# Kernel tuning notes

Hardware: AMD Instinct MI355X
Metric: run time of the kernel (lower is better)

The kernel has to match this reference:

```python
import jax, jax.numpy as jnp
import numpy as np

D_OUT, D_IN, R, N_TOK = 4096, 4096, 16, 8192

def setup_inputs() -> dict:
    key = jax.random.key(0)
    k1, k2, k3, k4 = jax.random.split(key, 4)
    x = jax.random.normal(k1, (N_TOK, D_IN), dtype=jnp.float32)
    W = jax.random.normal(k2, (D_OUT, D_IN), dtype=jnp.float32) * (1.0 / np.sqrt(D_IN))
    bias = jax.random.normal(k3, (D_OUT,), dtype=jnp.float32) * 0.02
    lora_B = jnp.zeros((D_OUT, R), dtype=jnp.float32)  # torch init: zeros
    lora_A = jax.random.normal(k4, (R, D_IN), dtype=jnp.float32) / R  # torch init: randn / r
    lora_scale = jnp.float32(1.0)
    return {"x": x, "W": W, "bias": bias, "lora_B": lora_B, "lora_A": lora_A, "lora_scale": lora_scale}

def reference(x, W, bias, lora_B, lora_A, lora_scale):
    # Faithful to torch: weight = W + scale * B @ A; out = x @ weight.T + bias
    weight = W + lora_scale * (lora_B @ lora_A)  # [d_out, d_in]
    return jnp.einsum('ni,oi->no', x, weight) + bias
```

## Files before the change

kernel.cpp:

```cpp
#include <hip/hip_runtime.h>
#include <stdint.h>
#include <stddef.h>

#define M_TOK 8192
#define N_OUT 4096
#define K_IN  4096
#define R_LORA 16
#define BM 128
#define BN 256
#define BK 32

#define WEFF_BLOCKS ((K_IN / 1024) * (N_OUT / 32))
#define CAST_BLOCKS ((M_TOK * K_IN) / (8 * 256))

typedef __bf16 bf16_t;
typedef __bf16 bf16x4 __attribute__((ext_vector_type(4)));
typedef __bf16 bf16x8 __attribute__((ext_vector_type(8)));
typedef float floatx4 __attribute__((ext_vector_type(4)));

__device__ inline void async_copy16(const bf16_t* g, bf16_t* l) {
  __builtin_amdgcn_global_load_lds(
      (__attribute__((address_space(1))) void*)(uintptr_t)(const void*)g,
      (__attribute__((address_space(3))) void*)l,
      16, 0, 0);
}

__global__ __launch_bounds__(256) void prep_fused(
    const float* __restrict__ x, bf16_t* __restrict__ xb,
    const float* __restrict__ W, const float* __restrict__ lB,
    const float* __restrict__ lA, const float* __restrict__ scale_p,
    bf16_t* __restrict__ wb) {
  const int b = blockIdx.x;
  if (b < WEFF_BLOCKS) {
    const int kbase = (b & 3) * 1024 + threadIdx.x * 4;
    const int o0    = (b >> 2) * 32;
    const float scale = *scale_p;

    float4 areg[R_LORA];
#pragma unroll
    for (int r = 0; r < R_LORA; ++r)
      areg[r] = *(const float4*)(lA + (size_t)r * K_IN + kbase);

    for (int oo = 0; oo < 32; ++oo) {
      const int o = o0 + oo;
      float4 w = *(const float4*)(W + (size_t)o * K_IN + kbase);
      float a0 = w.x, a1 = w.y, a2 = w.z, a3 = w.w;
#pragma unroll
      for (int r = 0; r < R_LORA; ++r) {
        float bb = lB[(size_t)o * R_LORA + r] * scale;
        a0 += bb * areg[r].x; a1 += bb * areg[r].y;
        a2 += bb * areg[r].z; a3 += bb * areg[r].w;
      }
      bf16x4 v;
      v[0] = (bf16_t)a0; v[1] = (bf16_t)a1; v[2] = (bf16_t)a2; v[3] = (bf16_t)a3;
      *(bf16x4*)(wb + (size_t)o * K_IN + kbase) = v;
    }
  } else {
    const size_t t = (size_t)(b - WEFF_BLOCKS) * 256 + threadIdx.x;
    const float4* xp = (const float4*)x + t * 2;
    float4 a0 = xp[0];
    float4 a1 = xp[1];
    bf16x8 v;
    v[0] = (bf16_t)a0.x; v[1] = (bf16_t)a0.y; v[2] = (bf16_t)a0.z; v[3] = (bf16_t)a0.w;
    v[4] = (bf16_t)a1.x; v[5] = (bf16_t)a1.y; v[6] = (bf16_t)a1.z; v[7] = (bf16_t)a1.w;
    *(bf16x8*)(xb + t * 8) = v;
  }
}

__global__ __launch_bounds__(256, 2) void gemm_bt(const bf16_t* __restrict__ A,
                                                  const bf16_t* __restrict__ Bw,
                                                  const float* __restrict__ bias,
                                                  float* __restrict__ C) {
  __shared__ bf16_t sA[2 * BM * BK];
  __shared__ bf16_t sB[2 * BN * BK];

  const int tid  = threadIdx.x;
  const int wave = tid >> 6;
  const int lane = tid & 63;
  const int lr   = lane & 15;
  const int quad = lane >> 4;
  const int bm = blockIdx.y * BM;
  const int bn = blockIdx.x * BN;
  const int wm = (wave >> 1) * 64;
  const int wn = (wave & 1) * 128;

  const bf16_t* gA[2];
  const bf16_t* gB[4];
  bf16_t* lA0[2];
  bf16_t* lB0[4];
#pragma unroll
  for (int i = 0; i < 2; ++i) {
    int s = i * 256 + wave * 64 + lane;
    int row = s >> 2;
    int q = ((s & 3) - (s >> 3)) & 3;
    gA[i] = A + (size_t)(bm + row) * K_IN + q * 8;
    lA0[i] = sA + (size_t)(i * 256 + wave * 64) * 8;
  }
#pragma unroll
  for (int i = 0; i < 4; ++i) {
    int s = i * 256 + wave * 64 + lane;
    int row = s >> 2;
    int q = ((s & 3) - (s >> 3)) & 3;
    gB[i] = Bw + (size_t)(bn + row) * K_IN + q * 8;
    lB0[i] = sB + (size_t)(i * 256 + wave * 64) * 8;
  }

  const int cofs = ((quad + (lr >> 1)) & 3) * 8;
  const bf16_t* fA[4];
  const bf16_t* fB[8];
#pragma unroll
  for (int i = 0; i < 4; ++i) fA[i] = sA + (wm + i * 16 + lr) * 32 + cofs;
#pragma unroll
  for (int j = 0; j < 8; ++j) fB[j] = sB + (wn + j * 16 + lr) * 32 + cofs;

  floatx4 acc[4][8];
#pragma unroll
  for (int i = 0; i < 4; ++i)
#pragma unroll
    for (int j = 0; j < 8; ++j) acc[i][j] = {0.f, 0.f, 0.f, 0.f};

#define STAGE(buf_ofsA, buf_ofsB)                                   \
  do {                                                              \
    async_copy16(gA[0], lA0[0] + (buf_ofsA));                       \
    async_copy16(gA[1], lA0[1] + (buf_ofsA));                       \
    async_copy16(gB[0], lB0[0] + (buf_ofsB));                       \
    async_copy16(gB[1], lB0[1] + (buf_ofsB));                       \
    async_copy16(gB[2], lB0[2] + (buf_ofsB));                       \
    async_copy16(gB[3], lB0[3] + (buf_ofsB));                       \
    gA[0] += BK; gA[1] += BK;                                       \
    gB[0] += BK; gB[1] += BK; gB[2] += BK; gB[3] += BK;             \
  } while (0)

#define COMPUTE(buf_ofsA, buf_ofsB)                                                   \
  do {                                                                                \
    bf16x8 a[4], b[8];                                                                \
    _Pragma("unroll") for (int i = 0; i < 4; ++i)                                     \
        a[i] = *(const bf16x8*)(fA[i] + (buf_ofsA));                                  \
    _Pragma("unroll") for (int j = 0; j < 8; ++j)                                     \
        b[j] = *(const bf16x8*)(fB[j] + (buf_ofsB));                                  \
    _Pragma("unroll") for (int i = 0; i < 4; ++i)                                     \
        _Pragma("unroll") for (int j = 0; j < 8; ++j)                                 \
            acc[i][j] = __builtin_amdgcn_mfma_f32_16x16x32_bf16(a[i], b[j],           \
                                                                acc[i][j], 0, 0, 0); \
  } while (0)

  STAGE(0, 0);
  for (int it = 0; it < K_IN / BK; it += 2) {
    __syncthreads();
    STAGE(BM * BK, BN * BK);
    COMPUTE(0, 0);
    __syncthreads();
    if (it + 2 < K_IN / BK) STAGE(0, 0);
    COMPUTE(BM * BK, BN * BK);
  }
#undef STAGE
#undef COMPUTE

#pragma unroll
  for (int j = 0; j < 8; ++j) {
    int col = bn + wn + j * 16 + lr;
    float bb = bias[col];
#pragma unroll
    for (int i = 0; i < 4; ++i) {
      int row0 = bm + wm + i * 16 + quad * 4;
      floatx4 v = acc[i][j];
#pragma unroll
      for (int r = 0; r < 4; ++r)
        C[(size_t)(row0 + r) * N_OUT + col] = v[r] + bb;
    }
  }
}

__global__ __launch_bounds__(256) void lora_xa(const float* __restrict__ x,
                                               const float* __restrict__ lA,
                                               const float* __restrict__ scale_p,
                                               float* __restrict__ t) {
  int m = blockIdx.x;
  int r = threadIdx.x & 15;
  int kcn = threadIdx.x >> 4;
  float acc = 0.f;
  const float* xr = x + (size_t)m * K_IN + kcn * 256;
  const float* ar = lA + (size_t)r * K_IN + kcn * 256;
  for (int k = 0; k < 256; k += 4) {
    float4 xv = *(const float4*)(xr + k);
    float4 av = *(const float4*)(ar + k);
    acc += xv.x * av.x + xv.y * av.y + xv.z * av.z + xv.w * av.w;
  }
  __shared__ float s[256];
  s[threadIdx.x] = acc;
  __syncthreads();
  if (threadIdx.x < 16) {
    float v = 0.f;
    for (int i = 0; i < 16; ++i) v += s[threadIdx.x + i * 16];
    t[(size_t)m * 16 + threadIdx.x] = v * (*scale_p);
  }
}

__global__ __launch_bounds__(256) void gemm_f32_fb(const float* __restrict__ X,
                                                   const float* __restrict__ W,
                                                   const float* __restrict__ bias,
                                                   const float* __restrict__ t,
                                                   const float* __restrict__ lB,
                                                   float* __restrict__ C) {
  __shared__ float sX[64][17];
  __shared__ float sW[64][17];
  int tid = threadIdx.x;
  int tx = tid & 15, ty = tid >> 4;
  int m0 = blockIdx.y * 64, n0 = blockIdx.x * 64;
  int lrow = tid >> 2, lcol = (tid & 3) * 4;
  float acc[4][4] = {};
  for (int k0 = 0; k0 < K_IN; k0 += 16) {
    __syncthreads();
    float4 xv = *(const float4*)(X + (size_t)(m0 + lrow) * K_IN + k0 + lcol);
    float4 wv = *(const float4*)(W + (size_t)(n0 + lrow) * K_IN + k0 + lcol);
    sX[lrow][lcol + 0] = xv.x; sX[lrow][lcol + 1] = xv.y;
    sX[lrow][lcol + 2] = xv.z; sX[lrow][lcol + 3] = xv.w;
    sW[lrow][lcol + 0] = wv.x; sW[lrow][lcol + 1] = wv.y;
    sW[lrow][lcol + 2] = wv.z; sW[lrow][lcol + 3] = wv.w;
    __syncthreads();
#pragma unroll
    for (int kk = 0; kk < 16; ++kk) {
      float xr[4], wr[4];
#pragma unroll
      for (int i = 0; i < 4; ++i) { xr[i] = sX[ty * 4 + i][kk]; wr[i] = sW[tx * 4 + i][kk]; }
#pragma unroll
      for (int i = 0; i < 4; ++i)
#pragma unroll
        for (int j = 0; j < 4; ++j) acc[i][j] += xr[i] * wr[j];
    }
  }
  for (int j = 0; j < 4; ++j) {
    int n = n0 + tx * 4 + j;
    float bb = bias[n];
    for (int i = 0; i < 4; ++i) {
      int m = m0 + ty * 4 + i;
      float l = 0.f;
      for (int r = 0; r < R_LORA; ++r) l += t[(size_t)m * 16 + r] * lB[(size_t)n * 16 + r];
      C[(size_t)m * N_OUT + n] = acc[i][j] + bb + l;
    }
  }
}

extern "C" void kernel_launch(void* const* d_in, const int* in_sizes, int n_in,
                              void* d_out, int out_size, void* d_ws, size_t ws_size,
                              hipStream_t stream) {
  const float* x     = (const float*)d_in[0];
  const float* W     = (const float*)d_in[1];
  const float* bias  = (const float*)d_in[2];
  const float* lB    = (const float*)d_in[3];
  const float* lA    = (const float*)d_in[4];
  const float* scale = (const float*)d_in[5];
  float* out = (float*)d_out;

  const size_t x_bytes = (size_t)M_TOK * K_IN * sizeof(bf16_t);
  const size_t w_bytes = (size_t)N_OUT * K_IN * sizeof(bf16_t);

  if (ws_size >= x_bytes + w_bytes) {
    bf16_t* xb = (bf16_t*)d_ws;
    bf16_t* wb = (bf16_t*)((char*)d_ws + x_bytes);
    prep_fused<<<WEFF_BLOCKS + CAST_BLOCKS, 256, 0, stream>>>(x, xb, W, lB, lA, scale, wb);
    gemm_bt<<<dim3(N_OUT / BN, M_TOK / BM), 256, 0, stream>>>(xb, wb, bias, out);
  } else {
    float* t = (float*)d_ws;
    lora_xa<<<M_TOK, 256, 0, stream>>>(x, lA, scale, t);
    gemm_f32_fb<<<dim3(N_OUT / 64, M_TOK / 64), 256, 0, stream>>>(x, W, bias, t, lB, out);
  }
}
```

Measured before the change: 556.9 us.

## Replace bf16 GEMM with 256x256x64 8-wave pipelined kernel and block swizzle

The bf16 GEMM is rewritten to use 256x256 output tiles with BK=64 and 512 threads (8 waves, each owning a 128x64 sub-tile). Global-to-LDS async copies are split into quarter stages interleaved with four MFMA quadrants, using explicit vmcnt/lgkmcnt waits, raw barriers, and s_setprio around MFMA bursts. The LDS layout uses an XOR swizzle to avoid bank conflicts, and a block-index swizzle groups tiles for L2 reuse. This aims at higher arithmetic intensity and better overlap of loads with MFMA. The cost is much more LDS per block (128KB), which may limit occupancy, plus fragile hand-written synchronisation.

```diff
diff --git a/kernel.cpp b/kernel.cpp
--- a/kernel.cpp
+++ b/kernel.cpp
@@ -6,9 +6,11 @@
 #define N_OUT 4096
 #define K_IN  4096
 #define R_LORA 16
-#define BM 128
+
+#define BM 256
 #define BN 256
-#define BK 32
+#define BK 64
+#define NT (K_IN / BK)
 
 #define WEFF_BLOCKS ((K_IN / 1024) * (N_OUT / 32))
 #define CAST_BLOCKS ((M_TOK * K_IN) / (8 * 256))
@@ -24,6 +26,12 @@
       (__attribute__((address_space(3))) void*)l,
       16, 0, 0);
 }
+
+#define BAR()   __builtin_amdgcn_s_barrier()
+#define VMCNT4  asm volatile("s_waitcnt vmcnt(4)" ::: "memory")
+#define VMCNT2  asm volatile("s_waitcnt vmcnt(2)" ::: "memory")
+#define VMCNT0  asm volatile("s_waitcnt vmcnt(0)" ::: "memory")
+#define LGKM0   asm volatile("s_waitcnt lgkmcnt(0)" ::: "memory")
 
 __global__ __launch_bounds__(256) void prep_fused(
     const float* __restrict__ x, bf16_t* __restrict__ xb,
@@ -67,106 +75,141 @@
   }
 }
 
-__global__ __launch_bounds__(256, 2) void gemm_bt(const bf16_t* __restrict__ A,
-                                                  const bf16_t* __restrict__ Bw,
-                                                  const float* __restrict__ bias,
-                                                  float* __restrict__ C) {
-  __shared__ bf16_t sA[2 * BM * BK];
-  __shared__ bf16_t sB[2 * BN * BK];
+__global__ __launch_bounds__(512, 2) void gemm_bt256(const bf16_t* __restrict__ A,
+                                                     const bf16_t* __restrict__ Bw,
+                                                     const float* __restrict__ bias,
+                                                     float* __restrict__ C) {
+  __shared__ bf16_t sA[2 * 2 * 128 * 64];
+  __shared__ bf16_t sB[2 * 2 * 128 * 64];
 
   const int tid  = threadIdx.x;
   const int wave = tid >> 6;
   const int lane = tid & 63;
   const int lr   = lane & 15;
   const int quad = lane >> 4;
-  const int bm = blockIdx.y * BM;
-  const int bn = blockIdx.x * BN;
-  const int wm = (wave >> 1) * 64;
-  const int wn = (wave & 1) * 128;
-
-  const bf16_t* gA[2];
-  const bf16_t* gB[4];
-  bf16_t* lA0[2];
-  bf16_t* lB0[4];
-#pragma unroll
-  for (int i = 0; i < 2; ++i) {
-    int s = i * 256 + wave * 64 + lane;
-    int row = s >> 2;
-    int q = ((s & 3) - (s >> 3)) & 3;
-    gA[i] = A + (size_t)(bm + row) * K_IN + q * 8;
-    lA0[i] = sA + (size_t)(i * 256 + wave * 64) * 8;
-  }
-#pragma unroll
-  for (int i = 0; i < 4; ++i) {
-    int s = i * 256 + wave * 64 + lane;
-    int row = s >> 2;
-    int q = ((s & 3) - (s >> 3)) & 3;
-    gB[i] = Bw + (size_t)(bn + row) * K_IN + q * 8;
-    lB0[i] = sB + (size_t)(i * 256 + wave * 64) * 8;
-  }
-
-  const int cofs = ((quad + (lr >> 1)) & 3) * 8;
-  const bf16_t* fA[4];
-  const bf16_t* fB[8];
-#pragma unroll
-  for (int i = 0; i < 4; ++i) fA[i] = sA + (wm + i * 16 + lr) * 32 + cofs;
-#pragma unroll
-  for (int j = 0; j < 8; ++j) fB[j] = sB + (wn + j * 16 + lr) * 32 + cofs;
-
-  floatx4 acc[4][8];
-#pragma unroll
-  for (int i = 0; i < 4; ++i)
-#pragma unroll
-    for (int j = 0; j < 8; ++j) acc[i][j] = {0.f, 0.f, 0.f, 0.f};
-
-#define STAGE(buf_ofsA, buf_ofsB)                                   \
-  do {                                                              \
-    async_copy16(gA[0], lA0[0] + (buf_ofsA));                       \
-    async_copy16(gA[1], lA0[1] + (buf_ofsA));                       \
-    async_copy16(gB[0], lB0[0] + (buf_ofsB));                       \
-    async_copy16(gB[1], lB0[1] + (buf_ofsB));                       \
-    async_copy16(gB[2], lB0[2] + (buf_ofsB));                       \
-    async_copy16(gB[3], lB0[3] + (buf_ofsB));                       \
-    gA[0] += BK; gA[1] += BK;                                       \
-    gB[0] += BK; gB[1] += BK; gB[2] += BK; gB[3] += BK;             \
-  } while (0)
-
-#define COMPUTE(buf_ofsA, buf_ofsB)                                                   \
-  do {                                                                                \
-    bf16x8 a[4], b[8];                                                                \
-    _Pragma("unroll") for (int i = 0; i < 4; ++i)                                     \
-        a[i] = *(const bf16x8*)(fA[i] + (buf_ofsA));                                  \
-    _Pragma("unroll") for (int j = 0; j < 8; ++j)                                     \
-        b[j] = *(const bf16x8*)(fB[j] + (buf_ofsB));                                  \
-    _Pragma("unroll") for (int i = 0; i < 4; ++i)                                     \
-        _Pragma("unroll") for (int j = 0; j < 8; ++j)                                 \
-            acc[i][j] = __builtin_amdgcn_mfma_f32_16x16x32_bf16(a[i], b[j],           \
-                                                                acc[i][j], 0, 0, 0); \
-  } while (0)
-
-  STAGE(0, 0);
-  for (int it = 0; it < K_IN / BK; it += 2) {
-    __syncthreads();
-    STAGE(BM * BK, BN * BK);
-    COMPUTE(0, 0);
-    __syncthreads();
-    if (it + 2 < K_IN / BK) STAGE(0, 0);
-    COMPUTE(BM * BK, BN * BK);
-  }
-#undef STAGE
-#undef COMPUTE
-
-#pragma unroll
-  for (int j = 0; j < 8; ++j) {
-    int col = bn + wn + j * 16 + lr;
-    float bb = bias[col];
-#pragma unroll
-    for (int i = 0; i < 4; ++i) {
-      int row0 = bm + wm + i * 16 + quad * 4;
-      floatx4 v = acc[i][j];
+  const int wr   = wave >> 2;
+  const int wc   = wave & 3;
+
+  const int bid = blockIdx.x;
+  const int swz = (bid & 7) * 64 + (bid >> 3);
+  const int bn  = (swz & 15) * BN;
+  const int bm  = (swz >> 4) * BM;
+
+  const int t8  = tid >> 3;
+  const int col = ((tid & 7) ^ (t8 & 7)) * 8;
+  const bf16_t* pA00 = A + (size_t)(bm +   0 + t8) * K_IN + col;
+  const bf16_t* pA01 = A + (size_t)(bm + 128 + t8) * K_IN + col;
+  const bf16_t* pA10 = A + (size_t)(bm +  64 + t8) * K_IN + col;
+  const bf16_t* pA11 = A + (size_t)(bm + 192 + t8) * K_IN + col;
+  const int brl = (t8 >> 5) * 64 + (t8 & 31);
+  const bf16_t* pB00 = Bw + (size_t)(bn +   0 + brl +  0) * K_IN + col;
+  const bf16_t* pB01 = Bw + (size_t)(bn + 128 + brl +  0) * K_IN + col;
+  const bf16_t* pB10 = Bw + (size_t)(bn +   0 + brl + 32) * K_IN + col;
+  const bf16_t* pB11 = Bw + (size_t)(bn + 128 + brl + 32) * K_IN + col;
+
+  const char* aR0 = (const char*)sA + (size_t)(wr * 64 + lr) * 128 + ((quad) ^ (lr & 7)) * 16;
+  const char* aR1 = (const char*)sA + (size_t)(wr * 64 + lr) * 128 + ((4 + quad) ^ (lr & 7)) * 16;
+  const char* bR0 = (const char*)sB + (size_t)(wc * 32 + lr) * 128 + ((quad) ^ (lr & 7)) * 16;
+  const char* bR1 = (const char*)sB + (size_t)(wc * 32 + lr) * 128 + ((4 + quad) ^ (lr & 7)) * 16;
+
+  floatx4 acc[8][4];
+#pragma unroll
+  for (int m = 0; m < 8; ++m)
+#pragma unroll
+    for (int n = 0; n < 4; ++n) acc[m][n] = {0.f, 0.f, 0.f, 0.f};
+
+#define STAGE_A0(nb) do { \
+    async_copy16(pA00, sA + (nb)         + wave * 512); \
+    async_copy16(pA01, sA + (nb) + 4096  + wave * 512); \
+    pA00 += BK; pA01 += BK; } while (0)
+#define STAGE_A1(nb) do { \
+    async_copy16(pA10, sA + (nb) + 8192  + wave * 512); \
+    async_copy16(pA11, sA + (nb) + 12288 + wave * 512); \
+    pA10 += BK; pA11 += BK; } while (0)
+#define STAGE_B0(nb) do { \
+    async_copy16(pB00, sB + (nb)         + wave * 512); \
+    async_copy16(pB01, sB + (nb) + 4096  + wave * 512); \
+    pB00 += BK; pB01 += BK; } while (0)
+#define STAGE_B1(nb) do { \
+    async_copy16(pB10, sB + (nb) + 8192  + wave * 512); \
+    async_copy16(pB11, sB + (nb) + 12288 + wave * 512); \
+    pB10 += BK; pB11 += BK; } while (0)
+
+#define READ_A(mh) do { _Pragma("unroll") for (int mm = 0; mm < 4; ++mm) { \
+    a[mm][0] = *(const bf16x8*)(aR0 + bufofs + (mh) * 16384 + mm * 2048); \
+    a[mm][1] = *(const bf16x8*)(aR1 + bufofs + (mh) * 16384 + mm * 2048); } } while (0)
+#define READ_B(nh) do { _Pragma("unroll") for (int nn = 0; nn < 2; ++nn) { \
+    b[(nh) * 2 + nn][0] = *(const bf16x8*)(bR0 + bufofs + (nh) * 16384 + nn * 2048); \
+    b[(nh) * 2 + nn][1] = *(const bf16x8*)(bR1 + bufofs + (nh) * 16384 + nn * 2048); } } while (0)
+
+#define MFMA_QUAD(mh, nh) do { \
+    __builtin_amdgcn_s_setprio(1); \
+    _Pragma("unroll") for (int mm = 0; mm < 4; ++mm) \
+    _Pragma("unroll") for (int nn = 0; nn < 2; ++nn) { \
+      acc[(mh)*4+mm][(nh)*2+nn] = __builtin_amdgcn_mfma_f32_16x16x32_bf16( \
+          a[mm][0], b[(nh)*2+nn][0], acc[(mh)*4+mm][(nh)*2+nn], 0, 0, 0); \
+      acc[(mh)*4+mm][(nh)*2+nn] = __builtin_amdgcn_mfma_f32_16x16x32_bf16( \
+          a[mm][1], b[(nh)*2+nn][1], acc[(mh)*4+mm][(nh)*2+nn], 0, 0, 0); } \
+    __builtin_amdgcn_s_setprio(0); } while (0)
+
+  STAGE_A0(0);
+  STAGE_B0(0);
+  STAGE_B1(0);
+  STAGE_A1(0);
+  VMCNT4;
+  BAR();
+
+  int bufofs = 0;
+  for (int t = 0; t < NT; ++t) {
+    const int nb = ((t + 1) & 1) * 16384;
+    const bool st = (t + 1 < NT);
+    bf16x8 a[4][2], b[4][2];
+
+    READ_A(0);
+    READ_B(0);
+    if (st) { STAGE_A0(nb); VMCNT4; } else { VMCNT2; }
+    BAR(); LGKM0;
+    MFMA_QUAD(0, 0);
+    BAR();
+
+    READ_B(1);
+    if (st) { STAGE_B0(nb); VMCNT4; } else { VMCNT0; }
+    BAR(); LGKM0;
+    MFMA_QUAD(0, 1);
+    BAR();
+
+    READ_A(1);
+    if (st) STAGE_B1(nb);
+    BAR(); LGKM0;
+    MFMA_QUAD(1, 1);
+    BAR();
+
+    if (st) { STAGE_A1(nb); VMCNT4; }
+    BAR(); LGKM0;
+    MFMA_QUAD(1, 0);
+    BAR();
+
+    bufofs ^= 32768;
+  }
+#undef STAGE_A0
+#undef STAGE_A1
+#undef STAGE_B0
+#undef STAGE_B1
+#undef READ_A
+#undef READ_B
+#undef MFMA_QUAD
+
+#pragma unroll
+  for (int n = 0; n < 4; ++n) {
+    const int colc = bn + wc * 64 + n * 16 + lr;
+    const float bb = bias[colc];
+#pragma unroll
+    for (int m = 0; m < 8; ++m) {
+      const int row0 = bm + wr * 128 + m * 16 + quad * 4;
+      floatx4 v = acc[m][n];
 #pragma unroll
       for (int r = 0; r < 4; ++r)
-        C[(size_t)(row0 + r) * N_OUT + col] = v[r] + bb;
+        C[(size_t)(row0 + r) * N_OUT + colc] = v[r] + bb;
     }
   }
 }
@@ -259,7 +302,7 @@
     bf16_t* xb = (bf16_t*)d_ws;
     bf16_t* wb = (bf16_t*)((char*)d_ws + x_bytes);
     prep_fused<<<WEFF_BLOCKS + CAST_BLOCKS, 256, 0, stream>>>(x, xb, W, lB, lA, scale, wb);
-    gemm_bt<<<dim3(N_OUT / BN, M_TOK / BM), 256, 0, stream>>>(xb, wb, bias, out);
+    gemm_bt256<<<(M_TOK / BM) * (N_OUT / BN), 512, 0, stream>>>(xb, wb, bias, out);
   } else {
     float* t = (float*)d_ws;
     lora_xa<<<M_TOK, 256, 0, stream>>>(x, lA, scale, t);
```

Result: no change. 566.1 us (+1.7%).
